# Kernel tuning notes

Measured on AMD Instinct MI355X. Metric: run time of the kernel, lower is better.

The kernel has to match this reference:

```python
import jax, jax.numpy as jnp
import numpy as np
from jax import lax


def setup_inputs() -> dict:
    key = jax.random.key(0)
    x = jax.random.normal(key, (16, 3, 1024, 1024), dtype=jnp.float32)
    return {"x": x, "kernel_size": 7}


def _box_conv(x, kernel, pad):
    # x: (B,1,H,W), kernel: (1,1,k,k); 'same' spatial conv
    return lax.conv_general_dilated(
        x, kernel,
        window_strides=(1, 1),
        padding=[(pad, pad), (pad, pad)],
        dimension_numbers=("NCHW", "OIHW", "NCHW"),
    )


def reference(x, kernel_size):
    k = kernel_size
    pad = k // 2
    # ConvertToLuminance: for 4D input, x.dim()==4 -> channel mean (not RGB weights)
    lum = jnp.mean(x, axis=1, keepdims=True)  # (B,1,H,W)
    kernel = jnp.ones((1, 1, k, k), dtype=x.dtype) / (k * k)
    mean = _box_conv(lum, kernel, pad)
    sqr_mean = _box_conv(lum * lum, kernel, pad)
    var = sqr_mean - mean * mean
    return var
```

## Files before the change

kernel.cpp:

```cpp
#include <hip/hip_runtime.h>

typedef float f4 __attribute__((ext_vector_type(4)));

#define Wd 1024
#define Hd 1024
#define SH 32
#define ITER (SH + 6)

__device__ __forceinline__ f4 load_lum(const float* __restrict__ x0,
                                       const float* __restrict__ x1,
                                       const float* __restrict__ x2, size_t o) {
    f4 a = *(const f4*)(x0 + o);
    f4 g = *(const f4*)(x1 + o);
    f4 c = *(const f4*)(x2 + o);
    return (a + g + c) * (1.f / 3.f);
}

__global__ __launch_bounds__(256, 4)
void lvm_stream(const float* __restrict__ x, float* __restrict__ out) {
    const int b    = blockIdx.y;
    const int row0 = blockIdx.x * SH;
    const int tid  = threadIdx.x;
    const int lane = tid & 63;
    const int c0   = tid * 4;

    const float* x0 = x + (size_t)b * 3 * Hd * Wd;
    const float* x1 = x0 + (size_t)Hd * Wd;
    const float* x2 = x1 + (size_t)Hd * Wd;
    float*       ob = out + (size_t)b * Hd * Wd;

    f4 ring1[7], ring2[7];

#pragma unroll
    for (int i = 0; i < ITER; ++i) {
        const int ri = row0 - 3 + i;
        const bool rv = (ri >= 0) && (ri < Hd);
        f4 lum = {0.f, 0.f, 0.f, 0.f};
        if (rv) lum = load_lum(x0, x1, x2, (size_t)ri * Wd + c0);

        float v1  = __shfl_up(lum.y, 1);
        float v2  = __shfl_up(lum.z, 1);
        float v3  = __shfl_up(lum.w, 1);
        float v8  = __shfl_down(lum.x, 1);
        float v9  = __shfl_down(lum.y, 1);
        float v10 = __shfl_down(lum.z, 1);

        if (lane == 0) {
            v1 = v2 = v3 = 0.f;
            if (rv && c0 >= 4) {
                f4 e = load_lum(x0, x1, x2, (size_t)ri * Wd + (c0 - 4));
                v1 = e.y; v2 = e.z; v3 = e.w;
            }
        }
        if (lane == 63) {
            v8 = v9 = v10 = 0.f;
            if (rv && (c0 + 4) < Wd) {
                f4 e = load_lum(x0, x1, x2, (size_t)ri * Wd + (c0 + 4));
                v8 = e.x; v9 = e.y; v10 = e.z;
            }
        }

        const float v4 = lum.x, v5 = lum.y, v6 = lum.z, v7 = lum.w;

        float s1a = v1 + v2 + v3 + v4 + v5 + v6 + v7;
        float s1b = s1a - v1 + v8;
        float s1c = s1b - v2 + v9;
        float s1d = s1c - v3 + v10;

        float q1 = v1 * v1, q2 = v2 * v2, q3 = v3 * v3, q4 = v4 * v4;
        float q5 = v5 * v5, q6 = v6 * v6, q7 = v7 * v7, q8 = v8 * v8;
        float q9 = v9 * v9, q10 = v10 * v10;
        float s2a = q1 + q2 + q3 + q4 + q5 + q6 + q7;
        float s2b = s2a - q1 + q8;
        float s2c = s2b - q2 + q9;
        float s2d = s2c - q3 + q10;

        ring1[i % 7] = (f4){s1a, s1b, s1c, s1d};
        ring2[i % 7] = (f4){s2a, s2b, s2c, s2d};

        if (i >= 6) {
            f4 t1 = ring1[0], t2 = ring2[0];
#pragma unroll
            for (int k = 1; k < 7; ++k) { t1 += ring1[k]; t2 += ring2[k]; }
            const float inv = 1.f / 49.f;
            f4 m = t1 * inv;
            f4 r = t2 * inv - m * m;
            const int ro = row0 + i - 6;
            __builtin_nontemporal_store(r, (f4*)(ob + (size_t)ro * Wd + c0));
        }
    }
}

extern "C" void kernel_launch(void* const* d_in, const int* in_sizes, int n_in,
                              void* d_out, int out_size, void* d_ws, size_t ws_size,
                              hipStream_t stream) {
    const float* x = (const float*)d_in[0];
    float* out = (float*)d_out;
    dim3 grid(Hd / SH, 16);
    lvm_stream<<<grid, dim3(256), 0, stream>>>(x, out);
}
```

Measured before the change: 319.0 us.

## Share luminance rows via LDS in batched chunks instead of wave shuffles

Each thread now loads several rows (CH=4) of luminance at once and writes them to a double-buffered LDS tile that spans the full row width plus zero padding. The horizontal halo is then read back from LDS, replacing the cross-lane shuffles and the extra global loads done by edge lanes. This is meant to remove divergent halo loads at wave boundaries and to get more loads in flight per thread. In exchange it adds a __syncthreads per chunk, about 33 KB of LDS per block that may cap occupancy, and more register pressure from holding four rows.

```diff
diff --git a/kernel.cpp b/kernel.cpp
--- a/kernel.cpp
+++ b/kernel.cpp
@@ -6,22 +6,16 @@
 #define Hd 1024
 #define SH 32
 #define ITER (SH + 6)
-
-__device__ __forceinline__ f4 load_lum(const float* __restrict__ x0,
-                                       const float* __restrict__ x1,
-                                       const float* __restrict__ x2, size_t o) {
-    f4 a = *(const f4*)(x0 + o);
-    f4 g = *(const f4*)(x1 + o);
-    f4 c = *(const f4*)(x2 + o);
-    return (a + g + c) * (1.f / 3.f);
-}
+#define CH 4
+#define NCH ((ITER + CH - 1) / CH)
 
 __global__ __launch_bounds__(256, 4)
 void lvm_stream(const float* __restrict__ x, float* __restrict__ out) {
+    __shared__ __align__(16) float L[2][CH][Wd + 8];
+
     const int b    = blockIdx.y;
     const int row0 = blockIdx.x * SH;
     const int tid  = threadIdx.x;
-    const int lane = tid & 63;
     const int c0   = tid * 4;
 
     const float* x0 = x + (size_t)b * 3 * Hd * Wd;
@@ -29,64 +23,84 @@
     const float* x2 = x1 + (size_t)Hd * Wd;
     float*       ob = out + (size_t)b * Hd * Wd;
 
+    if (tid < 4) {
+#pragma unroll
+        for (int p = 0; p < 2; ++p)
+#pragma unroll
+            for (int j = 0; j < CH; ++j) {
+                L[p][j][tid] = 0.f;
+                L[p][j][Wd + 4 + tid] = 0.f;
+            }
+    }
+
     f4 ring1[7], ring2[7];
 
 #pragma unroll
-    for (int i = 0; i < ITER; ++i) {
-        const int ri = row0 - 3 + i;
-        const bool rv = (ri >= 0) && (ri < Hd);
-        f4 lum = {0.f, 0.f, 0.f, 0.f};
-        if (rv) lum = load_lum(x0, x1, x2, (size_t)ri * Wd + c0);
+    for (int c = 0; c < NCH; ++c) {
+        const int buf = c & 1;
 
-        float v1  = __shfl_up(lum.y, 1);
-        float v2  = __shfl_up(lum.z, 1);
-        float v3  = __shfl_up(lum.w, 1);
-        float v8  = __shfl_down(lum.x, 1);
-        float v9  = __shfl_down(lum.y, 1);
-        float v10 = __shfl_down(lum.z, 1);
-
-        if (lane == 0) {
-            v1 = v2 = v3 = 0.f;
-            if (rv && c0 >= 4) {
-                f4 e = load_lum(x0, x1, x2, (size_t)ri * Wd + (c0 - 4));
-                v1 = e.y; v2 = e.z; v3 = e.w;
+        f4 lum[CH];
+#pragma unroll
+        for (int j = 0; j < CH; ++j) {
+            const int i = c * CH + j;
+            if (i < ITER) {
+                const int ri = row0 - 3 + i;
+                lum[j] = (f4){0.f, 0.f, 0.f, 0.f};
+                if (ri >= 0 && ri < Hd) {
+                    const size_t o = (size_t)ri * Wd + c0;
+                    f4 a  = *(const f4*)(x0 + o);
+                    f4 g  = *(const f4*)(x1 + o);
+                    f4 cc = *(const f4*)(x2 + o);
+                    lum[j] = (a + g + cc) * (1.f / 3.f);
+                }
             }
         }
-        if (lane == 63) {
-            v8 = v9 = v10 = 0.f;
-            if (rv && (c0 + 4) < Wd) {
-                f4 e = load_lum(x0, x1, x2, (size_t)ri * Wd + (c0 + 4));
-                v8 = e.x; v9 = e.y; v10 = e.z;
+#pragma unroll
+        for (int j = 0; j < CH; ++j) {
+            const int i = c * CH + j;
+            if (i < ITER) *(f4*)(&L[buf][j][4 + c0]) = lum[j];
+        }
+        __syncthreads();
+
+#pragma unroll
+        for (int j = 0; j < CH; ++j) {
+            const int i = c * CH + j;
+            if (i < ITER) {
+                const float* Lr = &L[buf][j][0];
+                f4 va = *(const f4*)(Lr + c0);
+                f4 vb = *(const f4*)(Lr + c0 + 4);
+                f4 vc = *(const f4*)(Lr + c0 + 8);
+                float v1 = va.y, v2 = va.z, v3 = va.w;
+                float v4 = vb.x, v5 = vb.y, v6 = vb.z, v7 = vb.w;
+                float v8 = vc.x, v9 = vc.y, v10 = vc.z;
+
+                float s1a = v1 + v2 + v3 + v4 + v5 + v6 + v7;
+                float s1b = s1a - v1 + v8;
+                float s1c = s1b - v2 + v9;
+                float s1d = s1c - v3 + v10;
+
+                float q1 = v1 * v1, q2 = v2 * v2, q3 = v3 * v3, q4 = v4 * v4;
+                float q5 = v5 * v5, q6 = v6 * v6, q7 = v7 * v7, q8 = v8 * v8;
+                float q9 = v9 * v9, q10 = v10 * v10;
+                float s2a = q1 + q2 + q3 + q4 + q5 + q6 + q7;
+                float s2b = s2a - q1 + q8;
+                float s2c = s2b - q2 + q9;
+                float s2d = s2c - q3 + q10;
+
+                ring1[i % 7] = (f4){s1a, s1b, s1c, s1d};
+                ring2[i % 7] = (f4){s2a, s2b, s2c, s2d};
+
+                if (i >= 6) {
+                    f4 t1 = ring1[0], t2 = ring2[0];
+#pragma unroll
+                    for (int k = 1; k < 7; ++k) { t1 += ring1[k]; t2 += ring2[k]; }
+                    const float inv = 1.f / 49.f;
+                    f4 m = t1 * inv;
+                    f4 r = t2 * inv - m * m;
+                    const int ro = row0 + i - 6;
+                    __builtin_nontemporal_store(r, (f4*)(ob + (size_t)ro * Wd + c0));
+                }
             }
-        }
-
-        const float v4 = lum.x, v5 = lum.y, v6 = lum.z, v7 = lum.w;
-
-        float s1a = v1 + v2 + v3 + v4 + v5 + v6 + v7;
-        float s1b = s1a - v1 + v8;
-        float s1c = s1b - v2 + v9;
-        float s1d = s1c - v3 + v10;
-
-        float q1 = v1 * v1, q2 = v2 * v2, q3 = v3 * v3, q4 = v4 * v4;
-        float q5 = v5 * v5, q6 = v6 * v6, q7 = v7 * v7, q8 = v8 * v8;
-        float q9 = v9 * v9, q10 = v10 * v10;
-        float s2a = q1 + q2 + q3 + q4 + q5 + q6 + q7;
-        float s2b = s2a - q1 + q8;
-        float s2c = s2b - q2 + q9;
-        float s2d = s2c - q3 + q10;
-
-        ring1[i % 7] = (f4){s1a, s1b, s1c, s1d};
-        ring2[i % 7] = (f4){s2a, s2b, s2c, s2d};
-
-        if (i >= 6) {
-            f4 t1 = ring1[0], t2 = ring2[0];
-#pragma unroll
-            for (int k = 1; k < 7; ++k) { t1 += ring1[k]; t2 += ring2[k]; }
-            const float inv = 1.f / 49.f;
-            f4 m = t1 * inv;
-            f4 r = t2 * inv - m * m;
-            const int ro = row0 + i - 6;
-            __builtin_nontemporal_store(r, (f4*)(ob + (size_t)ro * Wd + c0));
         }
     }
 }
```

After: 299.9 us. 1.06x faster.
